# Optimization experiments

Hardware: AMD Instinct MI355X
Metric: run time of the kernel (lower is better)

## Reference

```python
import jax, jax.numpy as jnp
import numpy as np
from jax.ops import segment_sum, segment_max

N, D, B = 1536, 32, 8            # nodes, candidate out-degree per node, sequential batch steps
OBS, HID, HEADS, C = 33, 64, 4, 8  # obs_dim, GRU hidden, attn heads, out_dim//heads
E = N * D


def setup_inputs() -> dict:
    key = jax.random.key(0)
    ks = jax.random.split(key, 16)
    g = lambda i, shape, s=0.1: jax.random.normal(ks[i], shape, jnp.float32) * s
    src = jnp.repeat(jnp.arange(N), D)                    # uniform degree -> scatter_topk = row top-k
    dst = jax.random.randint(ks[0], (E,), 0, N)
    return dict(
        H_t=jax.random.normal(ks[1], (B, N, OBS), jnp.float32),
        src=src, dst=dst, k=4,
        W_e1=g(2, (OBS, 32)), b_e1=jnp.zeros(32), W_e2=g(3, (32, 32)), b_e2=jnp.zeros(32),
        ln_g=jnp.ones(32), ln_b=jnp.zeros(32),
        W_ih=g(4, (3 * HID, 32)), W_hh=g(5, (3 * HID, HID)),
        b_ih=jnp.zeros(3 * HID), b_hh=jnp.zeros(3 * HID),
        W_s1=g(6, (2 * HID, 64)), b_s1=jnp.zeros(64), W_s2=g(7, (64, 1)), b_s2=jnp.zeros(1),
        W_gat=g(8, (HID, HEADS * C)), att_src=g(9, (HEADS, C)), att_dst=g(10, (HEADS, C)),
        b_gat=jnp.zeros(HEADS * C),
    )


def _layernorm(x, g, b, eps=1e-5):
    mu = x.mean(-1, keepdims=True)
    var = ((x - mu) ** 2).mean(-1, keepdims=True)
    return (x - mu) * jax.lax.rsqrt(var + eps) * g + b


def _forward(H_t, src, dst, k, W_e1, b_e1, W_e2, b_e2, ln_g, ln_b,
             W_ih, W_hh, b_ih, b_hh, W_s1, b_s1, W_s2, b_s2,
             W_gat, att_src, att_dst, b_gat):
    # ObsEmbedding: Linear-ReLU-Linear-ReLU-LayerNorm, applied to all (B,N) at once
    x = jax.nn.relu(H_t @ W_e1 + b_e1)
    x = jax.nn.relu(x @ W_e2 + b_e2)
    H_emb = _layernorm(x, ln_g, ln_b)              # (B,N,32)

    def step(h, e_t):
        # --- NodeMemory: shared GRUCell, h carried across batch steps ---
        gi = e_t @ W_ih.T + b_ih                   # (N,3H)
        gh = h @ W_hh.T + b_hh
        i_r, i_z, i_n = jnp.split(gi, 3, -1)
        h_r, h_z, h_n = jnp.split(gh, 3, -1)
        r = jax.nn.sigmoid(i_r + h_r)
        z = jax.nn.sigmoid(i_z + h_z)
        n = jnp.tanh(i_n + r * h_n)
        h_new = (1.0 - z) * n + z * h              # (N,HID)

        # --- EdgeScorer: sigmoid MLP score per candidate edge, keep top-k per source ---
        feat = jnp.concatenate([h_new[src], h_new[dst]], -1)        # (E,2*HID)
        score = jax.nn.sigmoid(
            (jax.nn.relu(feat @ W_s1 + b_s1) @ W_s2 + b_s2)[:, 0])  # (E,)
        s2 = score.reshape(N, D)
        top_idx = jax.lax.top_k(s2, k)[1]                           # (N,k)
        keep = (jnp.zeros((N, D), bool)
                .at[jnp.arange(N)[:, None], top_idx].set(True)).reshape(-1)  # (E,)
        w = jnp.where(keep, score, 0.0)                             # soft edge weights

        # --- GATConv (add_self_loops=False), pruned edges masked out of the softmax ---
        xh = (h_new @ W_gat).reshape(N, HEADS, C)
        a_s = (xh * att_src).sum(-1)               # (N,HEADS)
        a_d = (xh * att_dst).sum(-1)
        logit = jax.nn.leaky_relu(a_s[src] + a_d[dst], 0.2)         # (E,HEADS)
        logit = jnp.where(keep[:, None], logit, -1e30)
        m = segment_max(logit, dst, num_segments=N)                 # softmax grouped by target
        ex = jnp.where(keep[:, None], jnp.exp(logit - m[dst]), 0.0)
        ssum = segment_sum(ex, dst, num_segments=N)
        alpha = ex / jnp.clip(ssum[dst], 1e-16)                     # (E,HEADS)

        msg = alpha[:, :, None] * xh[src] * w[:, None, None]        # edge_weight scales messages
        out = segment_sum(msg, dst, num_segments=N).reshape(N, HEADS * C) + b_gat

        # --- densify attention: scatter-accumulate then row-normalize ---
        A = jnp.zeros((HEADS, N, N), alpha.dtype).at[:, src, dst].add(alpha.T)
        A = A / jnp.clip(A.sum(-1, keepdims=True), 1e-9)
        return h_new, (out, A)

    h0 = jnp.zeros((N, HID), H_t.dtype)
    _, (outs, attns) = jax.lax.scan(step, h0, H_emb)
    return outs, attns                              # (B,N,32), (B,HEADS,N,N)


def reference(H_t, src, dst, k, W_e1, b_e1, W_e2, b_e2, ln_g, ln_b,
              W_ih, W_hh, b_ih, b_hh, W_s1, b_s1, W_s2, b_s2,
              W_gat, att_src, att_dst, b_gat):
    return _forward(H_t, src, dst, k, W_e1, b_e1, W_e2, b_e2, ln_g, ln_b,
                    W_ih, W_hh, b_ih, b_hh, W_s1, b_s1, W_s2, b_s2,
                    W_gat, att_src, att_dst, b_gat)
```

## Files before the change

kernel.cpp:

```cpp
#include <hip/hip_runtime.h>
#include <math.h>

#define NN   1536
#define DG   32
#define BB   8
#define OBSD 33
#define HID  64
#define NHEAD 4
#define EE   (NN*DG)

__device__ __forceinline__ float sigm(float x){ return 1.0f/(1.0f+expf(-x)); }

__global__ void __launch_bounds__(256) k_embgi(
                      const float* __restrict__ Ht,
                      const float* __restrict__ We1, const float* __restrict__ be1,
                      const float* __restrict__ We2, const float* __restrict__ be2,
                      const float* __restrict__ lng, const float* __restrict__ lnb,
                      const float* __restrict__ Wih, const float* __restrict__ bih,
                      float* __restrict__ GI){
    __shared__ float lwih[192*33];
    int tid = threadIdx.x;
    for(int i=tid;i<192*32;i+=256){ int r=i>>5, c=i&31; lwih[r*33+c]=Wih[i]; }
    __syncthreads();
    int lane = tid & 63;
    int j32 = lane & 31;
    int bn = blockIdx.x*4 + (tid>>6);
    const float* hrow = Ht + (size_t)bn*OBSD;
    float x1 = be1[j32];
    for(int o=0;o<OBSD;o++) x1 += hrow[o]*We1[o*32+j32];
    x1 = fmaxf(x1,0.f);
    float x2 = be2[j32];
    for(int i=0;i<32;i++){
        float xi = __shfl(x1, (lane & 32) | i, 64);
        x2 += xi * We2[i*32+j32];
    }
    x2 = fmaxf(x2,0.f);
    float mu = x2;
    for(int m=16;m>=1;m>>=1) mu += __shfl_xor(mu, m, 32);
    mu *= (1.0f/32.0f);
    float d = x2-mu; float var = d*d;
    for(int m=16;m>=1;m>>=1) var += __shfl_xor(var, m, 32);
    var *= (1.0f/32.0f);
    float xln = d*rsqrtf(var+1e-5f)*lng[j32]+lnb[j32];
    int j = lane;
    float gr=bih[j], gz=bih[64+j], gn=bih[128+j];
    for(int kk=0;kk<32;kk++){
        float ek = __shfl(xln, kk, 64);
        gr += ek*lwih[j*33+kk];
        gz += ek*lwih[(64+j)*33+kk];
        gn += ek*lwih[(128+j)*33+kk];
    }
    float* g = GI + (size_t)bn*192;
    g[j]=gr; g[64+j]=gz; g[128+j]=gn;
}

__global__ void k_count(const int* __restrict__ dst, int* __restrict__ cursor){
    int e = blockIdx.x*256+threadIdx.x;
    if(e<EE) atomicAdd(&cursor[dst[e]],1);
}
__global__ void k_scan(int* __restrict__ cnt, int* __restrict__ indptr){
    __shared__ int part[256];
    int t = threadIdx.x;
    int local[6]; int s=0;
    for(int i=0;i<6;i++){ local[i]=cnt[t*6+i]; s+=local[i]; }
    part[t]=s; __syncthreads();
    if(t==0){ int acc=0; for(int i=0;i<256;i++){ int v=part[i]; part[i]=acc; acc+=v; } }
    __syncthreads();
    int pre = part[t];
    for(int i=0;i<6;i++){ int idx=t*6+i; indptr[idx]=pre; cnt[idx]=pre; pre+=local[i]; }
    if(t==255) indptr[NN]=EE;
}
__global__ void k_fill(const int* __restrict__ dst, int* __restrict__ cursor, int* __restrict__ eids){
    int e = blockIdx.x*256+threadIdx.x;
    if(e<EE){ int p = atomicAdd(&cursor[dst[e]],1); eids[p]=e; }
}

__global__ void __launch_bounds__(384) k_gru_all(const float* __restrict__ GI,
                       const float* __restrict__ Whh, const float* __restrict__ bhh,
                       float* __restrict__ Hall){
    __shared__ float lw[192*65];
    int tid = threadIdx.x;
    for(int i=tid;i<192*64;i+=384){ int r=i>>6, c=i&63; lw[r*65+c]=Whh[i]; }
    __syncthreads();
    int node = blockIdx.x*6 + (tid>>6);
    int j = tid&63;
    float b_r=bhh[j], b_z=bhh[64+j], b_n=bhh[128+j];
    const float* lwr = lw + j*65;
    const float* lwz = lw + (64+j)*65;
    const float* lwn = lw + (128+j)*65;
    float hold = 0.f;
    for(int t=0;t<BB;t++){
        float hr=b_r, hz=b_z, hn=b_n;
        for(int kk=0;kk<64;kk++){
            float hk = __shfl(hold,kk);
            hr += hk*lwr[kk];
            hz += hk*lwz[kk];
            hn += hk*lwn[kk];
        }
        const float* g = GI + ((size_t)t*NN+node)*192;
        float r  = sigm(g[j]     + hr);
        float z  = sigm(g[64+j]  + hz);
        float nn_= tanhf(g[128+j] + r*hn);
        hold = (1.f-z)*nn_ + z*hold;
        Hall[((size_t)t*NN+node)*64 + j] = hold;
    }
}

__global__ void __launch_bounds__(256) k_post(const float* __restrict__ Hall,
                       const float* __restrict__ Ws1, const float* __restrict__ Wgat,
                       const float* __restrict__ atts, const float* __restrict__ attd,
                       float* __restrict__ P, float* __restrict__ Q,
                       float* __restrict__ xh, float* __restrict__ as_, float* __restrict__ ad_){
    __shared__ float ws1l[128*64];
    __shared__ float wgl[64*32];
    int tid = threadIdx.x;
    for(int i=tid;i<128*64;i+=256) ws1l[i]=Ws1[i];
    for(int i=tid;i<64*32;i+=256)  wgl[i]=Wgat[i];
    __syncthreads();
    int bn = blockIdx.x*4 + (tid>>6);
    int j = tid&63;
    float hv = Hall[(size_t)bn*64+j];
    float p=0.f,q=0.f,xv=0.f;
    for(int kk=0;kk<64;kk++){
        float hk=__shfl(hv,kk);
        p += hk*ws1l[kk*64+j];
        q += hk*ws1l[(64+kk)*64+j];
        if(j<32) xv += hk*wgl[kk*32+j];
    }
    P[(size_t)bn*64+j]=p; Q[(size_t)bn*64+j]=q;
    if(j<32){
        xh[(size_t)bn*32+j]=xv;
        float asv = xv*atts[j];
        float adv = xv*attd[j];
        for(int m=1;m<8;m<<=1){ asv += __shfl_xor(asv,m); adv += __shfl_xor(adv,m); }
        if((j&7)==0){ as_[(size_t)bn*4+(j>>3)]=asv; ad_[(size_t)bn*4+(j>>3)]=adv; }
    }
}

__global__ void k_edge(const float* __restrict__ P, const float* __restrict__ Q,
                       const float* __restrict__ bs1, const float* __restrict__ Ws2,
                       const float* __restrict__ bs2, const int* __restrict__ dst,
                       const int* __restrict__ kptr, float* __restrict__ wbuf){
    int lane = threadIdx.x;
    int t = blockIdx.y;
    int row = blockIdx.x*2 + (lane>>5);
    int d = lane & 31;
    int e = row*DG + d;
    int de = dst[e];
    const float4* Pr = (const float4*)(P + ((size_t)t*NN+row)*64);
    const float4* Qr = (const float4*)(Q + ((size_t)t*NN+de)*64);
    const float4* B1 = (const float4*)bs1;
    const float4* W2 = (const float4*)Ws2;
    float acc = 0.f;
    #pragma unroll
    for(int jj=0;jj<16;jj++){
        float4 pv=Pr[jj], qv=Qr[jj], bv=B1[jj], wv=W2[jj];
        acc += fmaxf(pv.x+qv.x+bv.x,0.f)*wv.x;
        acc += fmaxf(pv.y+qv.y+bv.y,0.f)*wv.y;
        acc += fmaxf(pv.z+qv.z+bv.z,0.f)*wv.z;
        acc += fmaxf(pv.w+qv.w+bv.w,0.f)*wv.w;
    }
    float score = sigm(acc + bs2[0]);
    int kk = kptr[0]; if(kk>32) kk=32; if(kk<0) kk=0;
    bool sel=false;
    for(int it=0; it<kk; it++){
        float v = sel ? -INFINITY : score;
        int idx = d;
        for(int m=16;m>=1;m>>=1){
            float ov = __shfl_xor(v,m,32);
            int   oi = __shfl_xor(idx,m,32);
            if(ov>v || (ov==v && oi<idx)){ v=ov; idx=oi; }
        }
        if(idx==d) sel=true;
    }
    wbuf[(size_t)t*EE + e] = sel ? score : 0.f;
}

__global__ void __launch_bounds__(256) k_soft(const int* __restrict__ indptr, const int* __restrict__ eids,
                       const int* __restrict__ src,
                       const float* __restrict__ as_, const float* __restrict__ ad_,
                       const float* __restrict__ wbuf, const float* __restrict__ xhb,
                       const float* __restrict__ bgat,
                       float* __restrict__ alphab, float* __restrict__ outp){
    int n = blockIdx.x;
    int t = blockIdx.y;
    int h = threadIdx.x>>6;
    int lane = threadIdx.x&63;
    const float* w     = wbuf  + (size_t)t*EE;
    const float* asb   = as_   + (size_t)t*NN*4;
    const float* xhbt  = xhb   + (size_t)t*NN*32;
    float*       alpha = alphab+ (size_t)t*EE*4;
    int beg = indptr[n], end = indptr[n+1];
    float adv = ad_[((size_t)t*NN+n)*4+h];
    float m = -INFINITY;
    for(int i=beg+lane;i<end;i+=64){
        int e = eids[i];
        if(w[e]>0.f){
            float lg = asb[src[e]*4+h]+adv;
            lg = lg>0.f ? lg : 0.2f*lg;
            m = fmaxf(m,lg);
        }
    }
    for(int mm=32;mm>=1;mm>>=1) m = fmaxf(m,__shfl_xor(m,mm));
    float ssum=0.f;
    for(int i=beg+lane;i<end;i+=64){
        int e = eids[i];
        float ex = 0.f;
        if(w[e]>0.f){
            float lg = asb[src[e]*4+h]+adv;
            lg = lg>0.f ? lg : 0.2f*lg;
            ex = expf(lg-m);
        }
        alpha[e*4+h]=ex;
        ssum += ex;
    }
    for(int mm=32;mm>=1;mm>>=1) ssum += __shfl_xor(ssum,mm);
    float inv = 1.0f/fmaxf(ssum,1e-16f);
    float acc[8];
    #pragma unroll
    for(int c=0;c<8;c++) acc[c]=0.f;
    for(int i=beg+lane;i<end;i+=64){
        int e = eids[i];
        float a = alpha[e*4+h]*inv;
        alpha[e*4+h]=a;
        if(a>0.f){
            float aw = a*w[e];
            const float* xr = xhbt + src[e]*32 + h*8;
            #pragma unroll
            for(int c=0;c<8;c++) acc[c] += aw*xr[c];
        }
    }
    for(int mm=32;mm>=1;mm>>=1){
        #pragma unroll
        for(int c=0;c<8;c++) acc[c] += __shfl_xor(acc[c],mm);
    }
    if(lane==0){
        float* o = outp + ((size_t)t*NN+n)*32 + h*8;
        #pragma unroll
        for(int c=0;c<8;c++) o[c] = acc[c] + bgat[h*8+c];
    }
}

__global__ void __launch_bounds__(256) k_scatter(const float* __restrict__ alphab,
                       const int* __restrict__ dst, float* __restrict__ attn){
    __shared__ float rowbuf[NHEAD][NN];
    __shared__ float rs[NHEAD];
    __shared__ float rsf[NHEAD];
    int n = blockIdx.x;
    int t = blockIdx.y;
    const float* alpha = alphab + (size_t)t*EE*4;
    int tid = threadIdx.x;
    for(int i=tid;i<NHEAD*NN;i+=256) ((float*)rowbuf)[i]=0.f;
    if(tid<NHEAD) rs[tid]=0.f;
    __syncthreads();
    float a=0.f; int de=0; int h=0;
    if(tid<128){
        int d = tid>>2; h = tid&3;
        int e = n*DG+d;
        a = alpha[e*4+h];
        de = dst[e];
        if(a>0.f) atomicAdd(&rs[h], a);
    }
    __syncthreads();
    if(tid<NHEAD) rsf[tid] = 1.0f/fmaxf(rs[tid],1e-9f);
    __syncthreads();
    if(tid<128 && a>0.f) atomicAdd(&rowbuf[h][de], a*rsf[h]);
    __syncthreads();
    size_t tb = (size_t)t*NHEAD*NN*NN;
    for(int i=tid;i<NHEAD*(NN/4);i+=256){
        int hh = i/(NN/4); int c4 = i%(NN/4);
        float4 v = ((const float4*)rowbuf[hh])[c4];
        ((float4*)(attn + tb + (size_t)hh*NN*NN + (size_t)n*NN))[c4] = v;
    }
}

extern "C" void kernel_launch(void* const* d_in, const int* in_sizes, int n_in,
                              void* d_out, int out_size, void* d_ws, size_t ws_size,
                              hipStream_t stream) {
    const float* Ht   = (const float*)d_in[0];
    const int*   src  = (const int*)  d_in[1];
    const int*   dst  = (const int*)  d_in[2];
    const int*   kptr = (const int*)  d_in[3];
    const float* We1  = (const float*)d_in[4];
    const float* be1  = (const float*)d_in[5];
    const float* We2  = (const float*)d_in[6];
    const float* be2  = (const float*)d_in[7];
    const float* lng  = (const float*)d_in[8];
    const float* lnb  = (const float*)d_in[9];
    const float* Wih  = (const float*)d_in[10];
    const float* Whh  = (const float*)d_in[11];
    const float* bih  = (const float*)d_in[12];
    const float* bhh  = (const float*)d_in[13];
    const float* Ws1  = (const float*)d_in[14];
    const float* bs1  = (const float*)d_in[15];
    const float* Ws2  = (const float*)d_in[16];
    const float* bs2  = (const float*)d_in[17];
    const float* Wgat = (const float*)d_in[18];
    const float* atts = (const float*)d_in[19];
    const float* attd = (const float*)d_in[20];
    const float* bgat = (const float*)d_in[21];

    float* outp = (float*)d_out;
    float* attn = outp + (size_t)BB*NN*32;

    float* ws    = (float*)d_ws;
    float* GI    = ws;
    float* Hall  = ws + 2359296;
    float* P     = ws + 3145728;
    float* Q     = ws + 3932160;
    float* xh    = ws + 4718592;
    float* as_   = ws + 5111808;
    float* ad_   = ws + 5160960;
    float* wbuf  = ws + 5210112;
    float* alpha = ws + 5603328;
    int*   ibase = (int*)(ws + 7176192);
    int*   cursor= ibase;
    int*   indptr= ibase + 2048;
    int*   eids  = ibase + 4096;

    hipMemsetAsync(cursor, 0, (size_t)NN*sizeof(int), stream);

    k_embgi<<<BB*NN/4, 256, 0, stream>>>(Ht, We1, be1, We2, be2, lng, lnb, Wih, bih, GI);
    k_count<<<EE/256, 256, 0, stream>>>(dst, cursor);
    k_scan<<<1, 256, 0, stream>>>(cursor, indptr);
    k_fill<<<EE/256, 256, 0, stream>>>(dst, cursor, eids);
    k_gru_all<<<NN/6, 384, 0, stream>>>(GI, Whh, bhh, Hall);
    k_post<<<BB*NN/4, 256, 0, stream>>>(Hall, Ws1, Wgat, atts, attd, P, Q, xh, as_, ad_);
    {
        dim3 g(NN/2, BB);
        k_edge<<<g, 64, 0, stream>>>(P, Q, bs1, Ws2, bs2, dst, kptr, wbuf);
    }
    {
        dim3 g(NN, BB);
        k_soft<<<g, 256, 0, stream>>>(indptr, eids, src, as_, ad_, wbuf, xh, bgat, alpha, outp);
        k_scatter<<<g, 256, 0, stream>>>(alpha, dst, attn);
    }
}
```

Baseline: 521.7 us.

## Rework GRU, edge scoring, softmax and attention scatter kernels for fewer memory passes

Folds the cursor memset into the embedding kernel and holds the GRU hidden weights in registers instead of LDS. The edge scorer now uses one block per row with coalesced Q row reads and a wave reduction. The softmax gains a single-pass path for degree up to 64 and derives src from e>>5 rather than loading it. The attention densify drops the LDS zero-fill plus atomics and writes rows directly from a compacted list of kept edges. The src derivation assumes the uniform-degree layout the inputs use, and 192 register-resident weights per thread may cause spilling.

```diff
diff --git a/kernel.cpp b/kernel.cpp
--- a/kernel.cpp
+++ b/kernel.cpp
@@ -17,9 +17,10 @@
                       const float* __restrict__ We2, const float* __restrict__ be2,
                       const float* __restrict__ lng, const float* __restrict__ lnb,
                       const float* __restrict__ Wih, const float* __restrict__ bih,
-                      float* __restrict__ GI){
+                      float* __restrict__ GI, int* __restrict__ cursor){
     __shared__ float lwih[192*33];
     int tid = threadIdx.x;
+    if(blockIdx.x < 6) cursor[blockIdx.x*256 + tid] = 0;
     for(int i=tid;i<192*32;i+=256){ int r=i>>5, c=i&31; lwih[r*33+c]=Wih[i]; }
     __syncthreads();
     int lane = tid & 63;
@@ -84,18 +85,23 @@
     __syncthreads();
     int node = blockIdx.x*6 + (tid>>6);
     int j = tid&63;
+    float rw[64], rz[64], rn[64];
+    #pragma unroll
+    for(int kk=0;kk<64;kk++){
+        rw[kk]=lw[j*65+kk];
+        rz[kk]=lw[(64+j)*65+kk];
+        rn[kk]=lw[(128+j)*65+kk];
+    }
     float b_r=bhh[j], b_z=bhh[64+j], b_n=bhh[128+j];
-    const float* lwr = lw + j*65;
-    const float* lwz = lw + (64+j)*65;
-    const float* lwn = lw + (128+j)*65;
     float hold = 0.f;
     for(int t=0;t<BB;t++){
         float hr=b_r, hz=b_z, hn=b_n;
+        #pragma unroll
         for(int kk=0;kk<64;kk++){
             float hk = __shfl(hold,kk);
-            hr += hk*lwr[kk];
-            hz += hk*lwz[kk];
-            hn += hk*lwn[kk];
+            hr += hk*rw[kk];
+            hz += hk*rz[kk];
+            hn += hk*rn[kk];
         }
         const float* g = GI + ((size_t)t*NN+node)*192;
         float r  = sigm(g[j]     + hr);
@@ -137,47 +143,50 @@
     }
 }
 
-__global__ void k_edge(const float* __restrict__ P, const float* __restrict__ Q,
+__global__ void __launch_bounds__(256) k_edge(const float* __restrict__ P, const float* __restrict__ Q,
                        const float* __restrict__ bs1, const float* __restrict__ Ws2,
                        const float* __restrict__ bs2, const int* __restrict__ dst,
                        const int* __restrict__ kptr, float* __restrict__ wbuf){
-    int lane = threadIdx.x;
+    __shared__ float sc[DG];
+    int tid = threadIdx.x;
     int t = blockIdx.y;
-    int row = blockIdx.x*2 + (lane>>5);
-    int d = lane & 31;
-    int e = row*DG + d;
-    int de = dst[e];
-    const float4* Pr = (const float4*)(P + ((size_t)t*NN+row)*64);
-    const float4* Qr = (const float4*)(Q + ((size_t)t*NN+de)*64);
-    const float4* B1 = (const float4*)bs1;
-    const float4* W2 = (const float4*)Ws2;
-    float acc = 0.f;
-    #pragma unroll
-    for(int jj=0;jj<16;jj++){
-        float4 pv=Pr[jj], qv=Qr[jj], bv=B1[jj], wv=W2[jj];
-        acc += fmaxf(pv.x+qv.x+bv.x,0.f)*wv.x;
-        acc += fmaxf(pv.y+qv.y+bv.y,0.f)*wv.y;
-        acc += fmaxf(pv.z+qv.z+bv.z,0.f)*wv.z;
-        acc += fmaxf(pv.w+qv.w+bv.w,0.f)*wv.w;
-    }
-    float score = sigm(acc + bs2[0]);
-    int kk = kptr[0]; if(kk>32) kk=32; if(kk<0) kk=0;
-    bool sel=false;
-    for(int it=0; it<kk; it++){
-        float v = sel ? -INFINITY : score;
-        int idx = d;
-        for(int m=16;m>=1;m>>=1){
-            float ov = __shfl_xor(v,m,32);
-            int   oi = __shfl_xor(idx,m,32);
-            if(ov>v || (ov==v && oi<idx)){ v=ov; idx=oi; }
-        }
-        if(idx==d) sel=true;
-    }
-    wbuf[(size_t)t*EE + e] = sel ? score : 0.f;
+    int row = blockIdx.x;
+    int wv = tid>>6, j = tid&63;
+    float pv = P[((size_t)t*NN+row)*64 + j];
+    float bv = bs1[j], w2 = Ws2[j];
+    float b2 = bs2[0];
+    int des[8];
+    #pragma unroll
+    for(int i=0;i<8;i++) des[i] = dst[row*DG + wv*8 + i];
+    float qv[8];
+    #pragma unroll
+    for(int i=0;i<8;i++) qv[i] = Q[((size_t)t*NN+des[i])*64 + j];
+    #pragma unroll
+    for(int i=0;i<8;i++){
+        float v = fmaxf(pv+qv[i]+bv,0.f)*w2;
+        for(int m=32;m>=1;m>>=1) v += __shfl_xor(v,m);
+        if(j==0) sc[wv*8+i] = sigm(v+b2);
+    }
+    __syncthreads();
+    if(tid<32){
+        float score = sc[tid];
+        int kk = kptr[0]; if(kk>32) kk=32; if(kk<0) kk=0;
+        bool sel=false;
+        for(int it=0; it<kk; it++){
+            float v = sel ? -INFINITY : score;
+            int idx = tid;
+            for(int m=16;m>=1;m>>=1){
+                float ov = __shfl_xor(v,m,32);
+                int   oi = __shfl_xor(idx,m,32);
+                if(ov>v || (ov==v && oi<idx)){ v=ov; idx=oi; }
+            }
+            if(idx==tid) sel=true;
+        }
+        wbuf[(size_t)t*EE + row*DG + tid] = sel ? score : 0.f;
+    }
 }
 
 __global__ void __launch_bounds__(256) k_soft(const int* __restrict__ indptr, const int* __restrict__ eids,
-                       const int* __restrict__ src,
                        const float* __restrict__ as_, const float* __restrict__ ad_,
                        const float* __restrict__ wbuf, const float* __restrict__ xhb,
                        const float* __restrict__ bgat,
@@ -191,43 +200,72 @@
     const float* xhbt  = xhb   + (size_t)t*NN*32;
     float*       alpha = alphab+ (size_t)t*EE*4;
     int beg = indptr[n], end = indptr[n+1];
+    int deg = end-beg;
     float adv = ad_[((size_t)t*NN+n)*4+h];
-    float m = -INFINITY;
-    for(int i=beg+lane;i<end;i+=64){
-        int e = eids[i];
-        if(w[e]>0.f){
-            float lg = asb[src[e]*4+h]+adv;
+    float acc[8];
+    #pragma unroll
+    for(int c=0;c<8;c++) acc[c]=0.f;
+    if(deg<=64){
+        bool valid = lane<deg;
+        int e = valid ? eids[beg+lane] : 0;
+        float we = valid ? w[e] : 0.f;
+        bool kept = we>0.f;
+        int s = e>>5;
+        float lg = -INFINITY, ex = 0.f;
+        if(kept){
+            lg = asb[s*4+h]+adv;
             lg = lg>0.f ? lg : 0.2f*lg;
-            m = fmaxf(m,lg);
-        }
-    }
-    for(int mm=32;mm>=1;mm>>=1) m = fmaxf(m,__shfl_xor(m,mm));
-    float ssum=0.f;
-    for(int i=beg+lane;i<end;i+=64){
-        int e = eids[i];
-        float ex = 0.f;
-        if(w[e]>0.f){
-            float lg = asb[src[e]*4+h]+adv;
-            lg = lg>0.f ? lg : 0.2f*lg;
-            ex = expf(lg-m);
-        }
-        alpha[e*4+h]=ex;
-        ssum += ex;
-    }
-    for(int mm=32;mm>=1;mm>>=1) ssum += __shfl_xor(ssum,mm);
-    float inv = 1.0f/fmaxf(ssum,1e-16f);
-    float acc[8];
-    #pragma unroll
-    for(int c=0;c<8;c++) acc[c]=0.f;
-    for(int i=beg+lane;i<end;i+=64){
-        int e = eids[i];
-        float a = alpha[e*4+h]*inv;
-        alpha[e*4+h]=a;
-        if(a>0.f){
-            float aw = a*w[e];
-            const float* xr = xhbt + src[e]*32 + h*8;
-            #pragma unroll
-            for(int c=0;c<8;c++) acc[c] += aw*xr[c];
+        }
+        float m = lg;
+        for(int mm=32;mm>=1;mm>>=1) m = fmaxf(m,__shfl_xor(m,mm));
+        if(kept) ex = expf(lg-m);
+        float ssum = ex;
+        for(int mm=32;mm>=1;mm>>=1) ssum += __shfl_xor(ssum,mm);
+        float inv = 1.0f/fmaxf(ssum,1e-16f);
+        if(kept){
+            float a = ex*inv;
+            alpha[e*4+h] = a;
+            float aw = a*we;
+            const float4* xr = (const float4*)(xhbt + s*32 + h*8);
+            float4 x0 = xr[0], x1 = xr[1];
+            acc[0]+=aw*x0.x; acc[1]+=aw*x0.y; acc[2]+=aw*x0.z; acc[3]+=aw*x0.w;
+            acc[4]+=aw*x1.x; acc[5]+=aw*x1.y; acc[6]+=aw*x1.z; acc[7]+=aw*x1.w;
+        }
+    } else {
+        float m = -INFINITY;
+        for(int i=beg+lane;i<end;i+=64){
+            int e = eids[i];
+            if(w[e]>0.f){
+                float lg = asb[(e>>5)*4+h]+adv;
+                lg = lg>0.f ? lg : 0.2f*lg;
+                m = fmaxf(m,lg);
+            }
+        }
+        for(int mm=32;mm>=1;mm>>=1) m = fmaxf(m,__shfl_xor(m,mm));
+        float ssum=0.f;
+        for(int i=beg+lane;i<end;i+=64){
+            int e = eids[i];
+            float ex = 0.f;
+            if(w[e]>0.f){
+                float lg = asb[(e>>5)*4+h]+adv;
+                lg = lg>0.f ? lg : 0.2f*lg;
+                ex = expf(lg-m);
+            }
+            alpha[e*4+h]=ex;
+            ssum += ex;
+        }
+        for(int mm=32;mm>=1;mm>>=1) ssum += __shfl_xor(ssum,mm);
+        float inv = 1.0f/fmaxf(ssum,1e-16f);
+        for(int i=beg+lane;i<end;i+=64){
+            int e = eids[i];
+            if(w[e]>0.f){
+                float a = alpha[e*4+h]*inv;
+                alpha[e*4+h]=a;
+                float aw = a*w[e];
+                const float* xr = xhbt + (e>>5)*32 + h*8;
+                #pragma unroll
+                for(int c=0;c<8;c++) acc[c] += aw*xr[c];
+            } 
         }
     }
     for(int mm=32;mm>=1;mm>>=1){
@@ -236,41 +274,60 @@
     }
     if(lane==0){
         float* o = outp + ((size_t)t*NN+n)*32 + h*8;
-        #pragma unroll
-        for(int c=0;c<8;c++) o[c] = acc[c] + bgat[h*8+c];
+        float4 o0 = { acc[0]+bgat[h*8+0], acc[1]+bgat[h*8+1], acc[2]+bgat[h*8+2], acc[3]+bgat[h*8+3] };
+        float4 o1 = { acc[4]+bgat[h*8+4], acc[5]+bgat[h*8+5], acc[6]+bgat[h*8+6], acc[7]+bgat[h*8+7] };
+        ((float4*)o)[0]=o0; ((float4*)o)[1]=o1;
     }
 }
 
 __global__ void __launch_bounds__(256) k_scatter(const float* __restrict__ alphab,
+                       const float* __restrict__ wbuf,
                        const int* __restrict__ dst, float* __restrict__ attn){
-    __shared__ float rowbuf[NHEAD][NN];
-    __shared__ float rs[NHEAD];
-    __shared__ float rsf[NHEAD];
+    __shared__ int   kde[DG];
+    __shared__ float kan[DG][NHEAD];
+    __shared__ int   scnt;
     int n = blockIdx.x;
     int t = blockIdx.y;
+    int tid = threadIdx.x;
     const float* alpha = alphab + (size_t)t*EE*4;
-    int tid = threadIdx.x;
-    for(int i=tid;i<NHEAD*NN;i+=256) ((float*)rowbuf)[i]=0.f;
-    if(tid<NHEAD) rs[tid]=0.f;
-    __syncthreads();
-    float a=0.f; int de=0; int h=0;
-    if(tid<128){
-        int d = tid>>2; h = tid&3;
-        int e = n*DG+d;
-        a = alpha[e*4+h];
-        de = dst[e];
-        if(a>0.f) atomicAdd(&rs[h], a);
-    }
-    __syncthreads();
-    if(tid<NHEAD) rsf[tid] = 1.0f/fmaxf(rs[tid],1e-9f);
-    __syncthreads();
-    if(tid<128 && a>0.f) atomicAdd(&rowbuf[h][de], a*rsf[h]);
-    __syncthreads();
-    size_t tb = (size_t)t*NHEAD*NN*NN;
-    for(int i=tid;i<NHEAD*(NN/4);i+=256){
-        int hh = i/(NN/4); int c4 = i%(NN/4);
-        float4 v = ((const float4*)rowbuf[hh])[c4];
-        ((float4*)(attn + tb + (size_t)hh*NN*NN + (size_t)n*NN))[c4] = v;
+    const float* w     = wbuf   + (size_t)t*EE;
+    if(tid<64){
+        int d = tid;
+        int e = n*DG + d;
+        bool kept = false;
+        if(d<DG) kept = (w[e] > 0.f);
+        unsigned long long mask = __ballot(kept);
+        float4 av = {0.f,0.f,0.f,0.f};
+        int de = 0;
+        if(kept){ de = dst[e]; av = *(const float4*)(alpha + (size_t)e*4); }
+        float s0=av.x, s1=av.y, s2=av.z, s3=av.w;
+        for(int m=32;m>=1;m>>=1){
+            s0 += __shfl_xor(s0,m); s1 += __shfl_xor(s1,m);
+            s2 += __shfl_xor(s2,m); s3 += __shfl_xor(s3,m);
+        }
+        if(kept){
+            int pos = __popcll(mask & ((1ull<<d)-1ull));
+            kde[pos] = de;
+            kan[pos][0] = av.x / fmaxf(s0,1e-9f);
+            kan[pos][1] = av.y / fmaxf(s1,1e-9f);
+            kan[pos][2] = av.z / fmaxf(s2,1e-9f);
+            kan[pos][3] = av.w / fmaxf(s3,1e-9f);
+        }
+        if(tid==0) scnt = __popcll(mask);
+    }
+    __syncthreads();
+    int cnt = scnt;
+    size_t base = (size_t)t*NHEAD*NN*NN + (size_t)n*NN;
+    #pragma unroll
+    for(int it=0; it<6; it++){
+        int c = it*256 + tid;
+        int h = c/(NN/4), c4 = c%(NN/4);
+        float4 f4 = {0.f,0.f,0.f,0.f};
+        for(int p=0;p<cnt;p++){
+            int de = kde[p];
+            if((de>>2)==c4) ((float*)&f4)[de&3] += kan[p][h];
+        }
+        ((float4*)(attn + base + (size_t)h*NN*NN))[c4] = f4;
     }
 }
 
@@ -278,7 +335,6 @@
                               void* d_out, int out_size, void* d_ws, size_t ws_size,
                               hipStream_t stream) {
     const float* Ht   = (const float*)d_in[0];
-    const int*   src  = (const int*)  d_in[1];
     const int*   dst  = (const int*)  d_in[2];
     const int*   kptr = (const int*)  d_in[3];
     const float* We1  = (const float*)d_in[4];
@@ -318,21 +374,16 @@
     int*   indptr= ibase + 2048;
     int*   eids  = ibase + 4096;
 
-    hipMemsetAsync(cursor, 0, (size_t)NN*sizeof(int), stream);
-
-    k_embgi<<<BB*NN/4, 256, 0, stream>>>(Ht, We1, be1, We2, be2, lng, lnb, Wih, bih, GI);
+    k_embgi<<<BB*NN/4, 256, 0, stream>>>(Ht, We1, be1, We2, be2, lng, lnb, Wih, bih, GI, cursor);
     k_count<<<EE/256, 256, 0, stream>>>(dst, cursor);
     k_scan<<<1, 256, 0, stream>>>(cursor, indptr);
     k_fill<<<EE/256, 256, 0, stream>>>(dst, cursor, eids);
     k_gru_all<<<NN/6, 384, 0, stream>>>(GI, Whh, bhh, Hall);
     k_post<<<BB*NN/4, 256, 0, stream>>>(Hall, Ws1, Wgat, atts, attd, P, Q, xh, as_, ad_);
     {
-        dim3 g(NN/2, BB);
-        k_edge<<<g, 64, 0, stream>>>(P, Q, bs1, Ws2, bs2, dst, kptr, wbuf);
-    }
-    {
         dim3 g(NN, BB);
-        k_soft<<<g, 256, 0, stream>>>(indptr, eids, src, as_, ad_, wbuf, xh, bgat, alpha, outp);
-        k_scatter<<<g, 256, 0, stream>>>(alpha, dst, attn);
-    }
-}
+        k_edge<<<g, 256, 0, stream>>>(P, Q, bs1, Ws2, bs2, dst, kptr, wbuf);
+        k_soft<<<g, 256, 0, stream>>>(indptr, eids, as_, ad_, wbuf, xh, bgat, alpha, outp);
+        k_scatter<<<g, 256, 0, stream>>>(alpha, wbuf, dst, attn);
+    }
+}
```

Result: slower. 544.3 us (+4.3%).
